# Optimization experiments

Hardware: AMD Instinct MI355X
Metric: run time of the kernel (lower is better)

The kernel has to match this reference:

```python
import jax, jax.numpy as jnp
import numpy as np

N = 100000      # nodes
E = 1600000     # edges
F_IN = 64       # node_features
F_OUT = 32      # output_size


def _cheb2(H, row, col, w_norm, theta, bias):
    # ChebConv K=2, sym normalization, lambda_max=2 (GCLSTM default):
    # L_hat = L - I = -D^{-1/2} A D^{-1/2}, so T0 = H, T1 = -A_norm H
    agg = jax.ops.segment_sum(w_norm[:, None] * H[col], row, num_segments=N)  # [N, F_OUT]
    return H @ theta[0] - agg @ theta[1] + bias


def setup_inputs() -> dict:
    key = jax.random.key(0)
    ks = jax.random.split(key, 24)
    inp = {}
    inp["x"] = jax.random.normal(ks[0], (N, F_IN), jnp.float32)
    inp["edge_index"] = jax.random.randint(ks[1], (2, E), 0, N)
    inp["edge_weight"] = jax.random.uniform(ks[2], (E,), jnp.float32)
    inp["h"] = jax.random.normal(ks[3], (N, F_OUT), jnp.float32)
    inp["c"] = jax.random.normal(ks[4], (N, F_OUT), jnp.float32)
    s_in = float(1.0 / np.sqrt(F_IN))
    s_out = float(1.0 / np.sqrt(F_OUT))
    i = 5
    for g in "ifco":
        inp[f"W_{g}"] = jax.random.uniform(ks[i], (F_IN, F_OUT), jnp.float32, -s_in, s_in); i += 1
        inp[f"b_{g}"] = jax.random.uniform(ks[i], (1, F_OUT), jnp.float32, -s_in, s_in); i += 1
        inp[f"theta_{g}"] = jax.random.uniform(ks[i], (2, F_OUT, F_OUT), jnp.float32, -s_out, s_out); i += 1
        inp[f"cb_{g}"] = jax.random.uniform(ks[i], (F_OUT,), jnp.float32, -s_out, s_out); i += 1
    inp["W_lin"] = jax.random.uniform(ks[i], (F_OUT, 1), jnp.float32, -s_out, s_out); i += 1
    inp["b_lin"] = jax.random.uniform(ks[i], (1,), jnp.float32, -s_out, s_out)
    return inp


def reference(x, edge_index, edge_weight, h, c,
              W_i, b_i, theta_i, cb_i,
              W_f, b_f, theta_f, cb_f,
              W_c, b_c, theta_c, cb_c,
              W_o, b_o, theta_o, cb_o,
              W_lin, b_lin):
    row, col = edge_index[0], edge_index[1]
    # symmetric normalization of edge weights (get_laplacian 'sym')
    deg = jax.ops.segment_sum(edge_weight, row, num_segments=N)
    dis = jnp.where(deg > 0, jax.lax.rsqrt(jnp.where(deg > 0, deg, 1.0)), 0.0)
    w_norm = dis[row] * edge_weight * dis[col]  # [E]
    # GCLSTM gates: input x through dense W, hidden h through ChebConv
    I = jax.nn.sigmoid(x @ W_i + _cheb2(h, row, col, w_norm, theta_i, cb_i) + b_i)
    Fg = jax.nn.sigmoid(x @ W_f + _cheb2(h, row, col, w_norm, theta_f, cb_f) + b_f)
    T = jnp.tanh(x @ W_c + _cheb2(h, row, col, w_norm, theta_c, cb_c) + b_c)
    C = Fg * c + I * T
    O = jax.nn.sigmoid(x @ W_o + _cheb2(h, row, col, w_norm, theta_o, cb_o) + b_o)
    H = O * jnp.tanh(C)
    # wrapper head: relu then Linear(out, 1)
    return jax.nn.relu(H) @ W_lin + b_lin  # [N, 1]
```

## Files before the change

kernel.cpp:

```cpp
#include <hip/hip_runtime.h>
#include <math.h>

#define NN 100000
#define NE 1600000
#define EPB 8192
#define NEB 196
#define NBUK 391
#define CAP 8192

#define DEGSCALE 16777216.0f

typedef __attribute__((ext_vector_type(8))) short bf16x8;
typedef __attribute__((ext_vector_type(4))) float f32x4;

#define MFMA(A, B, C) __builtin_amdgcn_mfma_f32_16x16x32_bf16(A, B, C, 0, 0, 0)

__device__ __forceinline__ float sigm(float z) { return 1.0f / (1.0f + expf(-z)); }

__device__ __forceinline__ void split1(float v, unsigned short* hi, unsigned short* lo) {
  unsigned u = __float_as_uint(v);
  *hi = (unsigned short)(u >> 16);
  float hf = __uint_as_float(u & 0xFFFF0000u);
  float lf = v - hf;
  *lo = (unsigned short)(__float_as_uint(lf) >> 16);
}

__device__ __forceinline__ void split8(const float* f, bf16x8* hi, bf16x8* lo) {
#pragma unroll
  for (int j = 0; j < 8; ++j) {
    unsigned short h, l;
    split1(f[j], &h, &l);
    (*hi)[j] = (short)h;
    (*lo)[j] = (short)l;
  }
}

__device__ __forceinline__ bf16x8 as_bf16x8(uint4 q) {
  union { uint4 q; bf16x8 v; } u;
  u.q = q;
  return u.v;
}

__device__ __forceinline__ void load8(const float4* p, int idx4, float* f) {
  float4 a = p[idx4];
  float4 b = p[idx4 + 1];
  f[0] = a.x; f[1] = a.y; f[2] = a.z; f[3] = a.w;
  f[4] = b.x; f[5] = b.y; f[6] = b.z; f[7] = b.w;
}


__global__ __launch_bounds__(256) void k_p1(const int* __restrict__ row,
                                            int* __restrict__ counts) {
  __shared__ int hist[NBUK];
  for (int i = threadIdx.x; i < NBUK; i += 256) hist[i] = 0;
  __syncthreads();
  int e0 = blockIdx.x * EPB;
  int e1 = min(e0 + EPB, NE);
  for (int e = e0 + (int)threadIdx.x; e < e1; e += 256)
    atomicAdd(&hist[row[e] >> 8], 1);
  __syncthreads();
  for (int i = threadIdx.x; i < NBUK; i += 256)
    counts[blockIdx.x * NBUK + i] = hist[i];
}

__global__ __launch_bounds__(256) void k_s1(int* __restrict__ counts,
                                            int* __restrict__ total) {
  __shared__ int s[256];
  int b = blockIdx.x;
  int t = threadIdx.x;
  int v = (t < NEB) ? counts[t * NBUK + b] : 0;
  s[t] = v;
  __syncthreads();
  for (int o = 1; o < 256; o <<= 1) {
    int a = (t >= o) ? s[t - o] : 0;
    __syncthreads();
    s[t] += a;
    __syncthreads();
  }
  if (t < NEB) counts[t * NBUK + b] = s[t] - v;
  if (t == 255) total[b] = s[255];
}

struct S2PParams {
  const int* total;
  int* bases;
  const float* W[4];
  const float* T0[4];
  const float* T1[4];
  const float* b[4];
  const float* cb[4];
  uint4* fh;
  uint4* fl;
  float* bias;
};

__global__ __launch_bounds__(512) void k_s2p(S2PParams pp) {
  if (blockIdx.x == 0) {
    __shared__ int s[512];
    int t = threadIdx.x;
    int v = (t < NBUK) ? pp.total[t] : 0;
    s[t] = v;
    __syncthreads();
    for (int o = 1; o < 512; o <<= 1) {
      int a = (t >= o) ? s[t - o] : 0;
      __syncthreads();
      s[t] += a;
      __syncthreads();
    }
    if (t < NBUK) pp.bases[t] = s[t] - v;
    if (t == 0) pp.bases[NBUK] = NE;
    return;
  }
  int idx = (blockIdx.x - 1) * 512 + threadIdx.x;
  if (idx < 2048) {
    int T = idx >> 6;
    int lane = idx & 63;
    int ncol = ((T & 7) * 16) + (lane & 15);
    int g = ncol >> 5;
    int c = ncol & 31;
    int kq = (lane >> 4) * 8;
    const float* mat;
    int kbase;
    if (T < 16) { mat = pp.W[g]; kbase = (T >> 3) * 32 + kq; }
    else if (T < 24) { mat = pp.T0[g]; kbase = kq; }
    else { mat = pp.T1[g]; kbase = kq; }
    unsigned hw[4], lw[4];
#pragma unroll
    for (int jj = 0; jj < 4; ++jj) {
      unsigned short h0, l0, h1, l1;
      split1(mat[(kbase + 2 * jj) * 32 + c], &h0, &l0);
      split1(mat[(kbase + 2 * jj + 1) * 32 + c], &h1, &l1);
      hw[jj] = (unsigned)h0 | ((unsigned)h1 << 16);
      lw[jj] = (unsigned)l0 | ((unsigned)l1 << 16);
    }
    pp.fh[idx] = make_uint4(hw[0], hw[1], hw[2], hw[3]);
    pp.fl[idx] = make_uint4(lw[0], lw[1], lw[2], lw[3]);
  }
  if (blockIdx.x == 1 && threadIdx.x < 128) {
    int g = threadIdx.x >> 5;
    int c = threadIdx.x & 31;
    pp.bias[threadIdx.x] = pp.b[g][c] + pp.cb[g][c];
  }
}

__global__ __launch_bounds__(256) void k_p2(const int* __restrict__ row,
                                            const int* __restrict__ col,
                                            const float* __restrict__ ew,
                                            const int* __restrict__ rel,
                                            const int* __restrict__ bases,
                                            int2* __restrict__ colw) {
  __shared__ int cursor[NBUK];
  for (int i = threadIdx.x; i < NBUK; i += 256)
    cursor[i] = bases[i] + rel[blockIdx.x * NBUK + i];
  __syncthreads();
  int e0 = blockIdx.x * EPB;
  int e1 = min(e0 + EPB, NE);
  for (int e = e0 + (int)threadIdx.x; e < e1; e += 256) {
    int r = row[e];
    int c = col[e];
    float w = ew[e];
    int slot = atomicAdd(&cursor[r >> 8], 1);
    colw[slot] = make_int2(c | ((r & 255) << 17), __float_as_int(w));
  }
}

__global__ __launch_bounds__(256) void k_bucket(const int* __restrict__ bases,
                                               int2* __restrict__ colw,
                                               int* __restrict__ rowptr,
                                               float* __restrict__ dis) {
  __shared__ int2 stage[CAP];
  __shared__ int cnt[256], degfx[256], s[256], cursor[256];
  int b = blockIdx.x;
  int base = bases[b];
  int M = bases[b + 1] - base;
  if (M > CAP) M = CAP;
  int t = threadIdx.x;
  cnt[t] = 0;
  degfx[t] = 0;
  __syncthreads();
  for (int i = t; i < M; i += 256) {
    int2 e = colw[base + i];
    stage[i] = e;
    int rl = (e.x >> 17) & 255;
    atomicAdd(&cnt[rl], 1);
    unsigned fx = (unsigned)(__int_as_float(e.y) * DEGSCALE + 0.5f);
    atomicAdd((unsigned*)&degfx[rl], fx);
  }
  __syncthreads();
  int v = cnt[t];
  s[t] = v;
  __syncthreads();
  for (int o = 1; o < 256; o <<= 1) {
    int a = (t >= o) ? s[t - o] : 0;
    __syncthreads();
    s[t] += a;
    __syncthreads();
  }
  int excl = s[t] - v;
  int node = b * 256 + t;
  if (node <= NN) rowptr[node] = base + excl;
  if (node < NN) {
    unsigned fx = (unsigned)degfx[t];
    dis[node] = fx ? rsqrtf((float)fx * (1.0f / DEGSCALE)) : 0.0f;
  }
  cursor[t] = excl;
  __syncthreads();
  for (int i = t; i < M; i += 256) {
    int2 e = stage[i];
    int rl = (e.x >> 17) & 255;
    int r = atomicAdd(&cursor[rl], 1);
    colw[base + r] = e;
  }
}

struct FusedParams {
  const float4* x4;
  const float4* h4;
  const float* cst;
  const int* rowptr;
  const int2* colw;
  const float* dis;
  const uint4* fh;
  const uint4* fl;
  const float* bias;
  const float* wlin;
  const float* blin;
  float* out;
};

__global__ __launch_bounds__(256) void k_fused(FusedParams p) {
  const int lane = threadIdx.x & 63;
  const int wv = threadIdx.x >> 6;
  const int m0 = blockIdx.x * 64 + wv * 16;
  const int mr = lane & 15;
  const int quad = lane >> 4;
  int m = m0 + mr;
  if (m >= NN) m = NN - 1;

  bf16x8 xh[2], xl[2], hh, hl, gh, gl;
  float f[8];
#pragma unroll
  for (int kt = 0; kt < 2; ++kt) {
    load8(p.x4, (m * 64 + kt * 32 + quad * 8) >> 2, f);
    split8(f, &xh[kt], &xl[kt]);
  }
  load8(p.h4, (m * 32 + quad * 8) >> 2, f);
  split8(f, &hh, &hl);

  float fa[8] = {0.f, 0.f, 0.f, 0.f, 0.f, 0.f, 0.f, 0.f};
  float fb[8] = {0.f, 0.f, 0.f, 0.f, 0.f, 0.f, 0.f, 0.f};
  {
    int s0 = p.rowptr[m];
    int s1v = p.rowptr[m + 1];
    int j = s0;
    for (; j + 1 < s1v; j += 2) {
      int2 cw0 = p.colw[j];
      int2 cw1 = p.colw[j + 1];
      int c0 = cw0.x & 0x1FFFF;
      int c1 = cw1.x & 0x1FFFF;
      float w0 = __int_as_float(cw0.y) * p.dis[c0];
      float w1 = __int_as_float(cw1.y) * p.dis[c1];
      const float4* hp0 = p.h4 + c0 * 8 + quad * 2;
      const float4* hp1 = p.h4 + c1 * 8 + quad * 2;
      float4 a0 = hp0[0], a1 = hp0[1];
      float4 b0 = hp1[0], b1 = hp1[1];
      fa[0] = fmaf(w0, a0.x, fa[0]); fa[1] = fmaf(w0, a0.y, fa[1]);
      fa[2] = fmaf(w0, a0.z, fa[2]); fa[3] = fmaf(w0, a0.w, fa[3]);
      fa[4] = fmaf(w0, a1.x, fa[4]); fa[5] = fmaf(w0, a1.y, fa[5]);
      fa[6] = fmaf(w0, a1.z, fa[6]); fa[7] = fmaf(w0, a1.w, fa[7]);
      fb[0] = fmaf(w1, b0.x, fb[0]); fb[1] = fmaf(w1, b0.y, fb[1]);
      fb[2] = fmaf(w1, b0.z, fb[2]); fb[3] = fmaf(w1, b0.w, fb[3]);
      fb[4] = fmaf(w1, b1.x, fb[4]); fb[5] = fmaf(w1, b1.y, fb[5]);
      fb[6] = fmaf(w1, b1.z, fb[6]); fb[7] = fmaf(w1, b1.w, fb[7]);
    }
    if (j < s1v) {
      int2 cw0 = p.colw[j];
      int c0 = cw0.x & 0x1FFFF;
      float w0 = __int_as_float(cw0.y) * p.dis[c0];
      const float4* hp0 = p.h4 + c0 * 8 + quad * 2;
      float4 a0 = hp0[0], a1 = hp0[1];
      fa[0] = fmaf(w0, a0.x, fa[0]); fa[1] = fmaf(w0, a0.y, fa[1]);
      fa[2] = fmaf(w0, a0.z, fa[2]); fa[3] = fmaf(w0, a0.w, fa[3]);
      fa[4] = fmaf(w0, a1.x, fa[4]); fa[5] = fmaf(w0, a1.y, fa[5]);
      fa[6] = fmaf(w0, a1.z, fa[6]); fa[7] = fmaf(w0, a1.w, fa[7]);
    }
  }
  {
    float dn = -p.dis[m];
#pragma unroll
    for (int j = 0; j < 8; ++j) f[j] = dn * (fa[j] + fb[j]);
    split8(f, &gh, &gl);
  }

  float wl0 = p.wlin[mr];
  float wl1 = p.wlin[mr + 16];
  float bl = p.blin[0];

  f32x4 acc[8];
#pragma unroll 2
  for (int nt = 0; nt < 8; ++nt) {
    float bv = p.bias[nt * 16 + mr];
    f32x4 a;
    a[0] = bv; a[1] = bv; a[2] = bv; a[3] = bv;
    bf16x8 b0h = as_bf16x8(p.fh[nt * 64 + lane]);
    bf16x8 b0l = as_bf16x8(p.fl[nt * 64 + lane]);
    bf16x8 b1h = as_bf16x8(p.fh[(8 + nt) * 64 + lane]);
    bf16x8 b1l = as_bf16x8(p.fl[(8 + nt) * 64 + lane]);
    bf16x8 t0h = as_bf16x8(p.fh[(16 + nt) * 64 + lane]);
    bf16x8 t0l = as_bf16x8(p.fl[(16 + nt) * 64 + lane]);
    bf16x8 t1h = as_bf16x8(p.fh[(24 + nt) * 64 + lane]);
    bf16x8 t1l = as_bf16x8(p.fl[(24 + nt) * 64 + lane]);
    a = MFMA(xh[0], b0h, a); a = MFMA(xh[0], b0l, a); a = MFMA(xl[0], b0h, a);
    a = MFMA(xh[1], b1h, a); a = MFMA(xh[1], b1l, a); a = MFMA(xl[1], b1h, a);
    a = MFMA(hh, t0h, a);    a = MFMA(hh, t0l, a);    a = MFMA(hl, t0h, a);
    a = MFMA(gh, t1h, a);    a = MFMA(gh, t1l, a);    a = MFMA(gl, t1h, a);
    acc[nt] = a;
  }

#pragma unroll
  for (int r = 0; r < 4; ++r) {
    int node = m0 + quad * 4 + r;
    int nc = node < NN ? node : NN - 1;
    float c0 = p.cst[nc * 32 + mr];
    float c1 = p.cst[nc * 32 + 16 + mr];
    float I0 = sigm(acc[0][r]), I1 = sigm(acc[1][r]);
    float F0 = sigm(acc[2][r]), F1 = sigm(acc[3][r]);
    float T0 = tanhf(acc[4][r]), T1 = tanhf(acc[5][r]);
    float O0 = sigm(acc[6][r]), O1 = sigm(acc[7][r]);
    float C0 = fmaf(F0, c0, I0 * T0);
    float C1 = fmaf(F1, c1, I1 * T1);
    float H0 = O0 * tanhf(C0);
    float H1 = O1 * tanhf(C1);
    float part = fmaf(fmaxf(H0, 0.f), wl0, fmaxf(H1, 0.f) * wl1);
#pragma unroll
    for (int s = 1; s < 16; s <<= 1) part += __shfl_xor(part, s, 64);
    if (mr == 0 && node < NN) p.out[node] = part + bl;
  }
}

extern "C" void kernel_launch(void* const* d_in, const int* in_sizes, int n_in,
                              void* d_out, int out_size, void* d_ws, size_t ws_size,
                              hipStream_t stream) {
  const float* x = (const float*)d_in[0];
  const int* row = (const int*)d_in[1];
  const int* col = row + NE;
  const float* ew = (const float*)d_in[2];
  const float* h = (const float*)d_in[3];
  const float* c = (const float*)d_in[4];

  float* ws = (float*)d_ws;
  float* dis = ws;
  int* rowptr = (int*)(ws + 100000);
  int* counts = (int*)(ws + 200004);
  int* total = (int*)(ws + 276640);
  int* bases = (int*)(ws + 277032);
  uint4* fh = (uint4*)(ws + 277424);
  uint4* fl = (uint4*)(ws + 285616);
  float* biasws = ws + 293808;
  int2* colw = (int2*)(ws + 293936);

  k_p1<<<NEB, 256, 0, stream>>>(row, counts);
  k_s1<<<NBUK, 256, 0, stream>>>(counts, total);

  S2PParams sp;
  sp.total = total;
  sp.bases = bases;
  for (int g = 0; g < 4; ++g) {
    sp.W[g] = (const float*)d_in[5 + 4 * g];
    sp.b[g] = (const float*)d_in[6 + 4 * g];
    sp.T0[g] = (const float*)d_in[7 + 4 * g];
    sp.T1[g] = sp.T0[g] + 1024;
    sp.cb[g] = (const float*)d_in[8 + 4 * g];
  }
  sp.fh = fh;
  sp.fl = fl;
  sp.bias = biasws;
  k_s2p<<<9, 512, 0, stream>>>(sp);

  k_p2<<<NEB, 256, 0, stream>>>(row, col, ew, counts, bases, colw);
  k_bucket<<<NBUK, 256, 0, stream>>>(bases, colw, rowptr, dis);

  FusedParams fp;
  fp.x4 = (const float4*)x;
  fp.h4 = (const float4*)h;
  fp.cst = c;
  fp.rowptr = rowptr;
  fp.colw = colw;
  fp.dis = dis;
  fp.fh = fh;
  fp.fl = fl;
  fp.bias = biasws;
  fp.wlin = (const float*)d_in[21];
  fp.blin = (const float*)d_in[22];
  fp.out = (float*)d_out;
  k_fused<<<(NN + 63) / 64, 256, 0, stream>>>(fp);
}
```

Before: 250.8 us.

## Fuse CSR build passes into one cooperative kernel with grid syncs

```diff
diff --git a/kernel.cpp b/kernel.cpp
--- a/kernel.cpp
+++ b/kernel.cpp
@@ -1,12 +1,15 @@
 #include <hip/hip_runtime.h>
+#include <hip/hip_cooperative_groups.h>
 #include <math.h>
+
+namespace cg = cooperative_groups;
 
 #define NN 100000
 #define NE 1600000
-#define EPB 8192
-#define NEB 196
-#define NBUK 391
-#define CAP 8192
+#define GRID 782
+#define NBUK 782
+#define EPB2 2047
+#define CAP 2688
 
 #define DEGSCALE 16777216.0f
 
@@ -48,42 +51,16 @@
   f[4] = b.x; f[5] = b.y; f[6] = b.z; f[7] = b.w;
 }
 
-
-__global__ __launch_bounds__(256) void k_p1(const int* __restrict__ row,
-                                            int* __restrict__ counts) {
-  __shared__ int hist[NBUK];
-  for (int i = threadIdx.x; i < NBUK; i += 256) hist[i] = 0;
-  __syncthreads();
-  int e0 = blockIdx.x * EPB;
-  int e1 = min(e0 + EPB, NE);
-  for (int e = e0 + (int)threadIdx.x; e < e1; e += 256)
-    atomicAdd(&hist[row[e] >> 8], 1);
-  __syncthreads();
-  for (int i = threadIdx.x; i < NBUK; i += 256)
-    counts[blockIdx.x * NBUK + i] = hist[i];
-}
-
-__global__ __launch_bounds__(256) void k_s1(int* __restrict__ counts,
-                                            int* __restrict__ total) {
-  __shared__ int s[256];
-  int b = blockIdx.x;
-  int t = threadIdx.x;
-  int v = (t < NEB) ? counts[t * NBUK + b] : 0;
-  s[t] = v;
-  __syncthreads();
-  for (int o = 1; o < 256; o <<= 1) {
-    int a = (t >= o) ? s[t - o] : 0;
-    __syncthreads();
-    s[t] += a;
-    __syncthreads();
-  }
-  if (t < NEB) counts[t * NBUK + b] = s[t] - v;
-  if (t == 255) total[b] = s[255];
-}
-
-struct S2PParams {
-  const int* total;
+struct BuildParams {
+  const int* row;
+  const int* col;
+  const float* ew;
+  int* counts;
+  int* total;
   int* bases;
+  int2* colw;
+  int* rowptr;
+  float* dis;
   const float* W[4];
   const float* T0[4];
   const float* T1[4];
@@ -94,25 +71,66 @@
   float* bias;
 };
 
-__global__ __launch_bounds__(512) void k_s2p(S2PParams pp) {
-  if (blockIdx.x == 0) {
-    __shared__ int s[512];
-    int t = threadIdx.x;
-    int v = (t < NBUK) ? pp.total[t] : 0;
-    s[t] = v;
-    __syncthreads();
-    for (int o = 1; o < 512; o <<= 1) {
-      int a = (t >= o) ? s[t - o] : 0;
-      __syncthreads();
-      s[t] += a;
-      __syncthreads();
-    }
-    if (t < NBUK) pp.bases[t] = s[t] - v;
-    if (t == 0) pp.bases[NBUK] = NE;
-    return;
-  }
-  int idx = (blockIdx.x - 1) * 512 + threadIdx.x;
-  if (idx < 2048) {
+__global__ __launch_bounds__(256) void k_build(BuildParams bp) {
+  __shared__ int2 stage[CAP];
+  __shared__ int aux[640];
+  cg::grid_group grid = cg::this_grid();
+  const int b = blockIdx.x;
+  const int t = threadIdx.x;
+  int* sI = (int*)stage;
+
+  for (int i = t; i < NBUK; i += 256) sI[i] = 0;
+  __syncthreads();
+  {
+    int e0 = b * EPB2;
+    int e1 = min(e0 + EPB2, NE);
+    for (int e = e0 + t; e < e1; e += 256) atomicAdd(&sI[bp.row[e] >> 7], 1);
+  }
+  __syncthreads();
+  for (int i = t; i < NBUK; i += 256) bp.counts[b * NBUK + i] = sI[i];
+  grid.sync();
+
+  for (int k = t; k < NBUK; k += 256) sI[k] = bp.counts[k * NBUK + b];
+  __syncthreads();
+  {
+    int c0 = 4 * t;
+    int sum = 0;
+    int ce = min(c0 + 4, NBUK);
+    for (int k = c0; k < ce; ++k) sum += sI[k];
+    aux[t] = sum;
+    __syncthreads();
+    for (int o = 1; o < 256; o <<= 1) {
+      int a = (t >= o) ? aux[t - o] : 0;
+      __syncthreads();
+      aux[t] += a;
+      __syncthreads();
+    }
+    int run = aux[t] - sum;
+    for (int k = c0; k < ce; ++k) { int v = sI[k]; bp.counts[k * NBUK + b] = run; run += v; }
+    if (t == 255) bp.total[b] = run;
+  }
+  grid.sync();
+
+  if (b == 0) {
+    for (int k = t; k < NBUK; k += 256) sI[k] = bp.total[k];
+    __syncthreads();
+    int c0 = 4 * t;
+    int sum = 0;
+    int ce = min(c0 + 4, NBUK);
+    for (int k = c0; k < ce; ++k) sum += sI[k];
+    aux[t] = sum;
+    __syncthreads();
+    for (int o = 1; o < 256; o <<= 1) {
+      int a = (t >= o) ? aux[t - o] : 0;
+      __syncthreads();
+      aux[t] += a;
+      __syncthreads();
+    }
+    int run = aux[t] - sum;
+    for (int k = c0; k < ce; ++k) { bp.bases[k] = run; run += sI[k]; }
+    if (t == 255) bp.bases[NBUK] = NE;
+  } else if (b <= 8) {
+    int idx = (b - 1) * 256 + t;
     int T = idx >> 6;
     int lane = idx & 63;
     int ncol = ((T & 7) * 16) + (lane & 15);
@@ -121,9 +139,9 @@
     int kq = (lane >> 4) * 8;
     const float* mat;
     int kbase;
-    if (T < 16) { mat = pp.W[g]; kbase = (T >> 3) * 32 + kq; }
-    else if (T < 24) { mat = pp.T0[g]; kbase = kq; }
-    else { mat = pp.T1[g]; kbase = kq; }
+    if (T < 16) { mat = bp.W[g]; kbase = (T >> 3) * 32 + kq; }
+    else if (T < 24) { mat = bp.T0[g]; kbase = kq; }
+    else { mat = bp.T1[g]; kbase = kq; }
     unsigned hw[4], lw[4];
 #pragma unroll
     for (int jj = 0; jj < 4; ++jj) {
@@ -133,83 +151,76 @@
       hw[jj] = (unsigned)h0 | ((unsigned)h1 << 16);
       lw[jj] = (unsigned)l0 | ((unsigned)l1 << 16);
     }
-    pp.fh[idx] = make_uint4(hw[0], hw[1], hw[2], hw[3]);
-    pp.fl[idx] = make_uint4(lw[0], lw[1], lw[2], lw[3]);
-  }
-  if (blockIdx.x == 1 && threadIdx.x < 128) {
-    int g = threadIdx.x >> 5;
-    int c = threadIdx.x & 31;
-    pp.bias[threadIdx.x] = pp.b[g][c] + pp.cb[g][c];
-  }
-}
-
-__global__ __launch_bounds__(256) void k_p2(const int* __restrict__ row,
-                                            const int* __restrict__ col,
-                                            const float* __restrict__ ew,
-                                            const int* __restrict__ rel,
-                                            const int* __restrict__ bases,
-                                            int2* __restrict__ colw) {
-  __shared__ int cursor[NBUK];
-  for (int i = threadIdx.x; i < NBUK; i += 256)
-    cursor[i] = bases[i] + rel[blockIdx.x * NBUK + i];
+    bp.fh[idx] = make_uint4(hw[0], hw[1], hw[2], hw[3]);
+    bp.fl[idx] = make_uint4(lw[0], lw[1], lw[2], lw[3]);
+  } else if (b == 9 && t < 128) {
+    int g = t >> 5;
+    int c = t & 31;
+    bp.bias[t] = bp.b[g][c] + bp.cb[g][c];
+  }
+  grid.sync();
+
+  for (int i = t; i < NBUK; i += 256)
+    sI[i] = bp.bases[i] + bp.counts[b * NBUK + i];
   __syncthreads();
-  int e0 = blockIdx.x * EPB;
-  int e1 = min(e0 + EPB, NE);
-  for (int e = e0 + (int)threadIdx.x; e < e1; e += 256) {
-    int r = row[e];
-    int c = col[e];
-    float w = ew[e];
-    int slot = atomicAdd(&cursor[r >> 8], 1);
-    colw[slot] = make_int2(c | ((r & 255) << 17), __float_as_int(w));
-  }
-}
-
-__global__ __launch_bounds__(256) void k_bucket(const int* __restrict__ bases,
-                                               int2* __restrict__ colw,
-                                               int* __restrict__ rowptr,
-                                               float* __restrict__ dis) {
-  __shared__ int2 stage[CAP];
-  __shared__ int cnt[256], degfx[256], s[256], cursor[256];
-  int b = blockIdx.x;
-  int base = bases[b];
-  int M = bases[b + 1] - base;
-  if (M > CAP) M = CAP;
-  int t = threadIdx.x;
-  cnt[t] = 0;
-  degfx[t] = 0;
-  __syncthreads();
-  for (int i = t; i < M; i += 256) {
-    int2 e = colw[base + i];
-    stage[i] = e;
-    int rl = (e.x >> 17) & 255;
-    atomicAdd(&cnt[rl], 1);
-    unsigned fx = (unsigned)(__int_as_float(e.y) * DEGSCALE + 0.5f);
-    atomicAdd((unsigned*)&degfx[rl], fx);
-  }
-  __syncthreads();
-  int v = cnt[t];
-  s[t] = v;
-  __syncthreads();
-  for (int o = 1; o < 256; o <<= 1) {
-    int a = (t >= o) ? s[t - o] : 0;
-    __syncthreads();
-    s[t] += a;
-    __syncthreads();
-  }
-  int excl = s[t] - v;
-  int node = b * 256 + t;
-  if (node <= NN) rowptr[node] = base + excl;
-  if (node < NN) {
-    unsigned fx = (unsigned)degfx[t];
-    dis[node] = fx ? rsqrtf((float)fx * (1.0f / DEGSCALE)) : 0.0f;
-  }
-  cursor[t] = excl;
-  __syncthreads();
-  for (int i = t; i < M; i += 256) {
-    int2 e = stage[i];
-    int rl = (e.x >> 17) & 255;
-    int r = atomicAdd(&cursor[rl], 1);
-    colw[base + r] = e;
+  {
+    int e0 = b * EPB2;
+    int e1 = min(e0 + EPB2, NE);
+    for (int e = e0 + t; e < e1; e += 256) {
+      int r = bp.row[e];
+      int c = bp.col[e];
+      float w = bp.ew[e];
+      int slot = atomicAdd(&sI[r >> 7], 1);
+      bp.colw[slot] = make_int2(c | ((r & 127) << 17), __float_as_int(w));
+    }
+  }
+  grid.sync();
+
+  {
+    int base = bp.bases[b];
+    int M = bp.bases[b + 1] - base;
+    if (M > CAP) M = CAP;
+    int* cnt = aux;
+    int* degfx = aux + 128;
+    int* cur = aux + 256;
+    int* ss = aux + 384;
+    if (t < 128) { cnt[t] = 0; degfx[t] = 0; }
+    __syncthreads();
+    for (int i = t; i < M; i += 256) {
+      int2 e = bp.colw[base + i];
+      stage[i] = e;
+      int rl = (e.x >> 17) & 127;
+      atomicAdd(&cnt[rl], 1);
+      unsigned fx = (unsigned)(__int_as_float(e.y) * DEGSCALE + 0.5f);
+      atomicAdd((unsigned*)&degfx[rl], fx);
+    }
+    __syncthreads();
+    int v = (t < 128) ? cnt[t] : 0;
+    ss[t] = v;
+    __syncthreads();
+    for (int o = 1; o < 128; o <<= 1) {
+      int a = (t >= o) ? ss[t - o] : 0;
+      __syncthreads();
+      ss[t] += a;
+      __syncthreads();
+    }
+    if (t < 128) {
+      int excl = ss[t] - v;
+      int node = b * 128 + t;
+      if (node <= NN) bp.rowptr[node] = base + excl;
+      if (node < NN) {
+        unsigned fx = (unsigned)degfx[t];
+        bp.dis[node] = fx ? rsqrtf((float)fx * (1.0f / DEGSCALE)) : 0.0f;
+      }
+      cur[t] = excl;
+    }
+    __syncthreads();
+    for (int i = t; i < M; i += 256) {
+      int2 e = stage[i];
+      int rl = (e.x >> 17) & 127;
+      int r = atomicAdd(&cur[rl], 1);
+      bp.colw[base + r] = e;
+    }
   }
 }
 
@@ -253,36 +264,52 @@
     int s0 = p.rowptr[m];
     int s1v = p.rowptr[m + 1];
     int j = s0;
-    for (; j + 1 < s1v; j += 2) {
+    for (; j + 3 < s1v; j += 4) {
       int2 cw0 = p.colw[j];
       int2 cw1 = p.colw[j + 1];
-      int c0 = cw0.x & 0x1FFFF;
-      int c1 = cw1.x & 0x1FFFF;
+      int2 cw2 = p.colw[j + 2];
+      int2 cw3 = p.colw[j + 3];
+      int c0 = cw0.x & 0x1FFFF, c1 = cw1.x & 0x1FFFF;
+      int c2 = cw2.x & 0x1FFFF, c3 = cw3.x & 0x1FFFF;
       float w0 = __int_as_float(cw0.y) * p.dis[c0];
       float w1 = __int_as_float(cw1.y) * p.dis[c1];
+      float w2 = __int_as_float(cw2.y) * p.dis[c2];
+      float w3 = __int_as_float(cw3.y) * p.dis[c3];
       const float4* hp0 = p.h4 + c0 * 8 + quad * 2;
       const float4* hp1 = p.h4 + c1 * 8 + quad * 2;
-      float4 a0 = hp0[0], a1 = hp0[1];
-      float4 b0 = hp1[0], b1 = hp1[1];
-      fa[0] = fmaf(w0, a0.x, fa[0]); fa[1] = fmaf(w0, a0.y, fa[1]);
-      fa[2] = fmaf(w0, a0.z, fa[2]); fa[3] = fmaf(w0, a0.w, fa[3]);
-      fa[4] = fmaf(w0, a1.x, fa[4]); fa[5] = fmaf(w0, a1.y, fa[5]);
-      fa[6] = fmaf(w0, a1.z, fa[6]); fa[7] = fmaf(w0, a1.w, fa[7]);
-      fb[0] = fmaf(w1, b0.x, fb[0]); fb[1] = fmaf(w1, b0.y, fb[1]);
-      fb[2] = fmaf(w1, b0.z, fb[2]); fb[3] = fmaf(w1, b0.w, fb[3]);
-      fb[4] = fmaf(w1, b1.x, fb[4]); fb[5] = fmaf(w1, b1.y, fb[5]);
-      fb[6] = fmaf(w1, b1.z, fb[6]); fb[7] = fmaf(w1, b1.w, fb[7]);
-    }
-    if (j < s1v) {
+      const float4* hp2 = p.h4 + c2 * 8 + quad * 2;
+      const float4* hp3 = p.h4 + c3 * 8 + quad * 2;
+      float4 A0 = hp0[0], A1 = hp0[1];
+      float4 B0 = hp1[0], B1 = hp1[1];
+      float4 C0 = hp2[0], C1 = hp2[1];
+      float4 D0 = hp3[0], D1 = hp3[1];
+      fa[0] = fmaf(w0, A0.x, fa[0]); fa[1] = fmaf(w0, A0.y, fa[1]);
+      fa[2] = fmaf(w0, A0.z, fa[2]); fa[3] = fmaf(w0, A0.w, fa[3]);
+      fa[4] = fmaf(w0, A1.x, fa[4]); fa[5] = fmaf(w0, A1.y, fa[5]);
+      fa[6] = fmaf(w0, A1.z, fa[6]); fa[7] = fmaf(w0, A1.w, fa[7]);
+      fb[0] = fmaf(w1, B0.x, fb[0]); fb[1] = fmaf(w1, B0.y, fb[1]);
+      fb[2] = fmaf(w1, B0.z, fb[2]); fb[3] = fmaf(w1, B0.w, fb[3]);
+      fb[4] = fmaf(w1, B1.x, fb[4]); fb[5] = fmaf(w1, B1.y, fb[5]);
+      fb[6] = fmaf(w1, B1.z, fb[6]); fb[7] = fmaf(w1, B1.w, fb[7]);
+      fa[0] = fmaf(w2, C0.x, fa[0]); fa[1] = fmaf(w2, C0.y, fa[1]);
+      fa[2] = fmaf(w2, C0.z, fa[2]); fa[3] = fmaf(w2, C0.w, fa[3]);
+      fa[4] = fmaf(w2, C1.x, fa[4]); fa[5] = fmaf(w2, C1.y, fa[5]);
+      fa[6] = fmaf(w2, C1.z, fa[6]); fa[7] = fmaf(w2, C1.w, fa[7]);
+      fb[0] = fmaf(w3, D0.x, fb[0]); fb[1] = fmaf(w3, D0.y, fb[1]);
+      fb[2] = fmaf(w3, D0.z, fb[2]); fb[3] = fmaf(w3, D0.w, fb[3]);
+      fb[4] = fmaf(w3, D1.x, fb[4]); fb[5] = fmaf(w3, D1.y, fb[5]);
+      fb[6] = fmaf(w3, D1.z, fb[6]); fb[7] = fmaf(w3, D1.w, fb[7]);
+    }
+    for (; j < s1v; ++j) {
       int2 cw0 = p.colw[j];
       int c0 = cw0.x & 0x1FFFF;
       float w0 = __int_as_float(cw0.y) * p.dis[c0];
       const float4* hp0 = p.h4 + c0 * 8 + quad * 2;
-      float4 a0 = hp0[0], a1 = hp0[1];
-      fa[0] = fmaf(w0, a0.x, fa[0]); fa[1] = fmaf(w0, a0.y, fa[1]);
-      fa[2] = fmaf(w0, a0.z, fa[2]); fa[3] = fmaf(w0, a0.w, fa[3]);
-      fa[4] = fmaf(w0, a1.x, fa[4]); fa[5] = fmaf(w0, a1.y, fa[5]);
-      fa[6] = fmaf(w0, a1.z, fa[6]); fa[7] = fmaf(w0, a1.w, fa[7]);
+      float4 A0 = hp0[0], A1 = hp0[1];
+      fa[0] = fmaf(w0, A0.x, fa[0]); fa[1] = fmaf(w0, A0.y, fa[1]);
+      fa[2] = fmaf(w0, A0.z, fa[2]); fa[3] = fmaf(w0, A0.w, fa[3]);
+      fa[4] = fmaf(w0, A1.x, fa[4]); fa[5] = fmaf(w0, A1.y, fa[5]);
+      fa[6] = fmaf(w0, A1.z, fa[6]); fa[7] = fmaf(w0, A1.w, fa[7]);
     }
   }
   {
@@ -352,33 +379,37 @@
   float* dis = ws;
   int* rowptr = (int*)(ws + 100000);
   int* counts = (int*)(ws + 200004);
-  int* total = (int*)(ws + 276640);
-  int* bases = (int*)(ws + 277032);
-  uint4* fh = (uint4*)(ws + 277424);
-  uint4* fl = (uint4*)(ws + 285616);
-  float* biasws = ws + 293808;
-  int2* colw = (int2*)(ws + 293936);
-
-  k_p1<<<NEB, 256, 0, stream>>>(row, counts);
-  k_s1<<<NBUK, 256, 0, stream>>>(counts, total);
-
-  S2PParams sp;
-  sp.total = total;
-  sp.bases = bases;
+  int* total = (int*)(ws + 811528);
+  int* bases = (int*)(ws + 812312);
+  uint4* fh = (uint4*)(ws + 813096);
+  uint4* fl = (uint4*)(ws + 821288);
+  float* biasws = ws + 829480;
+  int2* colw = (int2*)(ws + 829608);
+
+  BuildParams bp;
+  bp.row = row;
+  bp.col = col;
+  bp.ew = ew;
+  bp.counts = counts;
+  bp.total = total;
+  bp.bases = bases;
+  bp.colw = colw;
+  bp.rowptr = rowptr;
+  bp.dis = dis;
   for (int g = 0; g < 4; ++g) {
-    sp.W[g] = (const float*)d_in[5 + 4 * g];
-    sp.b[g] = (const float*)d_in[6 + 4 * g];
-    sp.T0[g] = (const float*)d_in[7 + 4 * g];
-    sp.T1[g] = sp.T0[g] + 1024;
-    sp.cb[g] = (const float*)d_in[8 + 4 * g];
-  }
-  sp.fh = fh;
-  sp.fl = fl;
-  sp.bias = biasws;
-  k_s2p<<<9, 512, 0, stream>>>(sp);
-
-  k_p2<<<NEB, 256, 0, stream>>>(row, col, ew, counts, bases, colw);
-  k_bucket<<<NBUK, 256, 0, stream>>>(bases, colw, rowptr, dis);
+    bp.W[g] = (const float*)d_in[5 + 4 * g];
+    bp.b[g] = (const float*)d_in[6 + 4 * g];
+    bp.T0[g] = (const float*)d_in[7 + 4 * g];
+    bp.T1[g] = bp.T0[g] + 1024;
+    bp.cb[g] = (const float*)d_in[8 + 4 * g];
+  }
+  bp.fh = fh;
+  bp.fl = fl;
+  bp.bias = biasws;
+
+  void* args[] = {&bp};
+  hipLaunchCooperativeKernel((const void*)k_build, dim3(GRID), dim3(256), args,
+                             0, stream);
 
   FusedParams fp;
   fp.x4 = (const float4*)x;
```

New measurement: 667.3 us. +166.1%, slower.
